# Kernel tuning notes

Measured on AMD Instinct MI355X. Metric: run time of the kernel, lower is better.

The kernel has to match this reference:

```python
import jax, jax.numpy as jnp
import numpy as np

B, S, H, I, E = 2, 2048, 1024, 4096, 8
NUM_STEPS = 2
RMS_EPS = 1e-6


def rmsnorm(x, w, eps=RMS_EPS):
    var = jnp.mean(jnp.square(x), axis=-1, keepdims=True)
    return x * jax.lax.rsqrt(var + eps) * w


def setup_inputs() -> dict:
    key = jax.random.key(0)
    ks = jax.random.split(key, 7)
    return {
        "hidden_states": jax.random.normal(ks[0], (B, S, H), dtype=jnp.float32),
        "gate_w": jax.random.normal(ks[1], (E, H), dtype=jnp.float32) * 0.02,
        "w1": jax.random.normal(ks[2], (E, H, I), dtype=jnp.float32) * 0.02,
        "b1": jnp.zeros((E, I), dtype=jnp.float32),
        "w2": jax.random.normal(ks[3], (E, I, H), dtype=jnp.float32) * 0.02,
        "b2": jnp.zeros((E, H), dtype=jnp.float32),
        "ln_w": jnp.ones((H,), dtype=jnp.float32),
    }


def reference(hidden_states, gate_w, w1, b1, w2, b2, ln_w):
    x = hidden_states  # [B,S,H]
    dtype = hidden_states.dtype
    for i in range(NUM_STEPS):
        inp = x if i == 0 else rmsnorm(x, ln_w)
        t = inp.reshape(-1, H)  # [T,H], T = B*S
        # softmax gate (computed in fp32 as in the original)
        logits = t @ gate_w.T  # [T,E]
        rw = jax.nn.softmax(logits.astype(jnp.float32), axis=-1).astype(dtype)
        # all experts on all tokens (dense MoE), batched over E
        h = jax.nn.silu(jnp.einsum('td,edi->tei', t, w1) + b1)  # [T,E,I]
        eo = jnp.einsum('tei,eih->teh', h, w2) + b2             # [T,E,H]
        comb = jnp.einsum('te,teh->th', rw, eo)                 # weighted combine
        x = x + comb.reshape(B, S, H)
    return x  # final_projection is Identity (no feature extractor)
```

## Files before the change

### kernel.cpp

```cpp
#include <hip/hip_runtime.h>
#include <hip/hip_bf16.h>

#define T_TOK 4096
#define H_DIM 1024
#define I_DIM 4096
#define E_EXP 8
#define RMS_EPS_F 1e-6f

using bf16x8 = __attribute__((ext_vector_type(8))) __bf16;
using f32x4  = __attribute__((ext_vector_type(4))) float;

__device__ inline void gload_lds16(const void* g, void* l) {
    __builtin_amdgcn_global_load_lds(
        (const __attribute__((address_space(1))) void*)g,
        (__attribute__((address_space(3))) void*)l,
        16, 0, 0);
}

__global__ __launch_bounds__(256) void k_transpose_cvt(
    const float* __restrict__ in, __hip_bfloat16* __restrict__ out, int R, int C)
{
    __shared__ float tile[32][33];
    const size_t mat = (size_t)R * C;
    in  += (size_t)blockIdx.z * mat;
    out += (size_t)blockIdx.z * mat;
    const int c0 = blockIdx.x * 32, r0 = blockIdx.y * 32;
    const int tx = threadIdx.x & 31, ty = threadIdx.x >> 5;
#pragma unroll
    for (int dy = 0; dy < 32; dy += 8)
        tile[ty + dy][tx] = in[(size_t)(r0 + ty + dy) * C + (c0 + tx)];
    __syncthreads();
#pragma unroll
    for (int dy = 0; dy < 32; dy += 8)
        out[(size_t)(c0 + ty + dy) * R + (r0 + tx)] = __float2bfloat16(tile[tx][ty + dy]);
}

__global__ __launch_bounds__(256) void k_prep(
    const float* __restrict__ x, const float* __restrict__ lnw,
    __hip_bfloat16* __restrict__ tb, int do_norm)
{
    const int t = blockIdx.x;
    const float* row = x + (size_t)t * H_DIM;
    const int base = threadIdx.x * 4;
    float4 v = *(const float4*)(row + base);
    if (do_norm) {
        float ss = v.x*v.x + v.y*v.y + v.z*v.z + v.w*v.w;
#pragma unroll
        for (int off = 32; off > 0; off >>= 1) ss += __shfl_xor(ss, off);
        __shared__ float wsum[4];
        const int w = threadIdx.x >> 6;
        if ((threadIdx.x & 63) == 0) wsum[w] = ss;
        __syncthreads();
        const float tot = wsum[0] + wsum[1] + wsum[2] + wsum[3];
        const float scale = rsqrtf(tot * (1.0f / H_DIM) + RMS_EPS_F);
        float4 g = *(const float4*)(lnw + base);
        v.x *= scale * g.x; v.y *= scale * g.y; v.z *= scale * g.z; v.w *= scale * g.w;
    }
    __hip_bfloat16* o = tb + (size_t)t * H_DIM + base;
    o[0] = __float2bfloat16(v.x); o[1] = __float2bfloat16(v.y);
    o[2] = __float2bfloat16(v.z); o[3] = __float2bfloat16(v.w);
}

__global__ __launch_bounds__(256) void k_gate(
    const __hip_bfloat16* __restrict__ tb, const float* __restrict__ gw,
    float* __restrict__ rw)
{
    const int t = blockIdx.x * 4 + (threadIdx.x >> 6);
    const int lane = threadIdx.x & 63;
    const __hip_bfloat16* row = tb + (size_t)t * H_DIM;
    float acc[E_EXP];
#pragma unroll
    for (int e = 0; e < E_EXP; ++e) acc[e] = 0.f;
    for (int h = lane; h < H_DIM; h += 64) {
        const float xv = __bfloat162float(row[h]);
#pragma unroll
        for (int e = 0; e < E_EXP; ++e) acc[e] += xv * gw[e * H_DIM + h];
    }
#pragma unroll
    for (int e = 0; e < E_EXP; ++e) {
#pragma unroll
        for (int off = 32; off > 0; off >>= 1) acc[e] += __shfl_xor(acc[e], off);
    }
    if (lane == 0) {
        float mx = acc[0];
#pragma unroll
        for (int e = 1; e < E_EXP; ++e) mx = fmaxf(mx, acc[e]);
        float ex[E_EXP], s = 0.f;
#pragma unroll
        for (int e = 0; e < E_EXP; ++e) { ex[e] = __expf(acc[e] - mx); s += ex[e]; }
        const float inv = 1.f / s;
#pragma unroll
        for (int e = 0; e < E_EXP; ++e) rw[(size_t)t * E_EXP + e] = ex[e] * inv;
    }
}


template<int BB, int MBASE>
__device__ __forceinline__ void ld_a4(bf16x8 (&a)[4], const char* rdA, int kof) {
#pragma unroll
    for (int mi = 0; mi < 4; ++mi)
        a[mi] = *(const bf16x8*)(rdA + BB * 32768 + (MBASE + mi) * 2048 + kof);
}
template<int BB>
__device__ __forceinline__ void ld_b4(bf16x8 (&b)[4], const char* rdB, int kof) {
#pragma unroll
    for (int ni = 0; ni < 4; ++ni)
        b[ni] = *(const bf16x8*)(rdB + BB * 32768 + ni * 2048 + kof);
}
template<int MB>
__device__ __forceinline__ void mfma_cell(const bf16x8 (&a)[4], const bf16x8 (&b)[4],
                                          f32x4 (&acc)[8][4]) {
    __builtin_amdgcn_s_setprio(1);
#pragma unroll
    for (int mi = 0; mi < 4; ++mi)
#pragma unroll
        for (int ni = 0; ni < 4; ++ni)
            acc[MB + mi][ni] = __builtin_amdgcn_mfma_f32_16x16x32_bf16(
                a[mi], b[ni], acc[MB + mi][ni], 0, 0, 0);
    __builtin_amdgcn_s_setprio(0);
}

#define BAR()   __builtin_amdgcn_s_barrier()
#define LGKM0() asm volatile("s_waitcnt lgkmcnt(0)" ::: "memory")
#define VMW(n)  asm volatile("s_waitcnt vmcnt(" #n ")" ::: "memory")
#define SCHED0() __builtin_amdgcn_sched_barrier(0)

template <int MODE>
__global__ __launch_bounds__(512, 2) void k_gemm8(
    const __hip_bfloat16* __restrict__ A, int lda, long long strideA,
    const __hip_bfloat16* __restrict__ Bt, int ldb, long long strideB,
    const float* __restrict__ bias, int strideBias,
    const float* __restrict__ rw, int e0,
    void* __restrict__ out, int ldo, long long strideOut, int K)
{
    __shared__ __hip_bfloat16 sA[2][2][128 * 64];
    __shared__ __hip_bfloat16 sB[2][2][128 * 64];

    const int z = blockIdx.z;
    A  += (size_t)z * (size_t)strideA;
    Bt += (size_t)z * (size_t)strideB;

    const int tid  = threadIdx.x;
    const int lane = tid & 63;
    const int wid  = tid >> 6;
    const int wr = wid >> 2, wc = wid & 3;
    const int m0 = blockIdx.y * 256, n0 = blockIdx.x * 256;

    const int sr  = tid >> 3;
    const int skb = ((((tid & 7) * 16) ^ ((sr & 7) << 4)) >> 1);
    const __hip_bfloat16* gA = A  + (size_t)(m0 + sr) * lda + skb;
    const __hip_bfloat16* gB = Bt + (size_t)(n0 + sr) * ldb + skb;
    char* const dA = (char*)&sA[0][0][0] + tid * 16;
    char* const dB = (char*)&sB[0][0][0] + tid * 16;

#define STAGE_A(bb, hh, kt) do { \
    const __hip_bfloat16* s_ = gA + (size_t)(hh) * 128 * lda + (size_t)(kt) * 64; \
    gload_lds16(s_,                     dA + (bb) * 32768 + (hh) * 16384); \
    gload_lds16(s_ + (size_t)64 * lda,  dA + (bb) * 32768 + (hh) * 16384 + 8192); \
} while (0)
#define STAGE_B(bb, hh, kt) do { \
    const __hip_bfloat16* s_ = gB + (size_t)(hh) * 128 * ldb + (size_t)(kt) * 64; \
    gload_lds16(s_,                     dB + (bb) * 32768 + (hh) * 16384); \
    gload_lds16(s_ + (size_t)64 * ldb,  dB + (bb) * 32768 + (hh) * 16384 + 8192); \
} while (0)

    const int fr = lane & 15, kg = lane >> 4;
    const int msk  = (fr & 7) << 4;
    const int kof0 = (kg * 16) ^ msk;
    const int kof1 = (64 + kg * 16) ^ msk;
    const char* rdA = (const char*)&sA[0][wr][0] + fr * 128;
    const char* rdB = (const char*)&sB[0][wc >> 1][0] + (wc & 1) * 8192 + fr * 128;

    f32x4  acc[8][4] = {};
    bf16x8 a[4], b[4], a2[4], a2n[4], bn[4];

    const int NT = K >> 6;

    STAGE_B(0, 0, 0); STAGE_B(0, 1, 0);
    STAGE_A(0, 0, 0); STAGE_A(0, 1, 0);
    STAGE_B(1, 0, 1); STAGE_B(1, 1, 1);
    VMW(4); BAR(); SCHED0();

#define TILE_PIPE(BB, t) do { \
     \
    ld_a4<BB, 0>(a, rdA, kof0); \
    ld_b4<BB>(b, rdB, kof0); \
    STAGE_A((BB) ^ 1, 0, (t) + 1); \
    LGKM0(); SCHED0(); \
    ld_a4<BB, 4>(a2, rdA, kof0);             \
    SCHED0(); \
    mfma_cell<0>(a, b, acc); \
     \
    STAGE_A((BB) ^ 1, 1, (t) + 1); \
    LGKM0(); SCHED0(); \
    ld_a4<BB, 4>(a2n, rdA, kof1);            \
    ld_b4<BB>(bn, rdB, kof1); \
    SCHED0(); \
    mfma_cell<4>(a2, b, acc); \
    BAR();                                    \
     \
    LGKM0(); SCHED0(); \
    ld_a4<BB, 0>(a, rdA, kof1);              \
    SCHED0(); \
    STAGE_B(BB, 0, (t) + 2); \
    mfma_cell<4>(a2n, bn, acc); \
     \
    LGKM0(); SCHED0(); \
    STAGE_B(BB, 1, (t) + 2); \
    mfma_cell<0>(a, bn, acc); \
    VMW(4); BAR(); SCHED0(); \
} while (0)

    for (int i = 0; i < NT / 2 - 1; ++i) {
        TILE_PIPE(0, 2 * i);
        TILE_PIPE(1, 2 * i + 1);
    }
    {
        ld_a4<0, 0>(a, rdA, kof0);
        ld_b4<0>(b, rdB, kof0);
        STAGE_A(1, 0, NT - 1);
        LGKM0(); SCHED0();
        ld_a4<0, 4>(a2, rdA, kof0);
        SCHED0();
        mfma_cell<0>(a, b, acc);
        STAGE_A(1, 1, NT - 1);
        LGKM0(); SCHED0();
        ld_a4<0, 4>(a2n, rdA, kof1);
        ld_b4<0>(bn, rdB, kof1);
        SCHED0();
        mfma_cell<4>(a2, b, acc);
        BAR();
        LGKM0(); SCHED0();
        ld_a4<0, 0>(a, rdA, kof1);
        SCHED0();
        mfma_cell<4>(a2n, bn, acc);
        LGKM0(); SCHED0();
        mfma_cell<0>(a, bn, acc);
        VMW(0); BAR(); SCHED0();
        ld_a4<1, 0>(a, rdA, kof0);
        ld_b4<1>(b, rdB, kof0);
        LGKM0(); SCHED0();
        ld_a4<1, 4>(a2, rdA, kof0);
        SCHED0();
        mfma_cell<0>(a, b, acc);
        LGKM0(); SCHED0();
        ld_a4<1, 4>(a2n, rdA, kof1);
        ld_b4<1>(bn, rdB, kof1);
        SCHED0();
        mfma_cell<4>(a2, b, acc);
        LGKM0(); SCHED0();
        ld_a4<1, 0>(a, rdA, kof1);
        SCHED0();
        mfma_cell<4>(a2n, bn, acc);
        LGKM0(); SCHED0();
        mfma_cell<0>(a, bn, acc);
    }

    const int rB = kg * 4;
    if (MODE == 0) {
        __hip_bfloat16* O = (__hip_bfloat16*)out + (size_t)z * (size_t)strideOut;
        const float* bz = bias + (size_t)z * (size_t)strideBias;
#pragma unroll
        for (int mi = 0; mi < 8; ++mi) {
            const int gm = m0 + wr * 128 + mi * 16 + rB;
#pragma unroll
            for (int j = 0; j < 4; ++j) {
                const int row = gm + j;
                const float rwv = rw[(size_t)row * E_EXP + e0 + z];
#pragma unroll
                for (int ni = 0; ni < 4; ++ni) {
                    const int gn = n0 + wc * 64 + ni * 16 + fr;
                    float v = acc[mi][ni][j] + bz[gn];
                    v = v / (1.f + __expf(-v));
                    O[(size_t)row * ldo + gn] = __float2bfloat16(rwv * v);
                }
            }
        }
    } else {
        __hip_bfloat16* O = (__hip_bfloat16*)out + (size_t)z * (size_t)strideOut;
#pragma unroll
        for (int mi = 0; mi < 8; ++mi) {
            const int gm = m0 + wr * 128 + mi * 16 + rB;
#pragma unroll
            for (int ni = 0; ni < 4; ++ni) {
                const int gn = n0 + wc * 64 + ni * 16 + fr;
#pragma unroll
                for (int j = 0; j < 4; ++j)
                    O[(size_t)(gm + j) * ldo + gn] = __float2bfloat16(acc[mi][ni][j]);
            }
        }
    }
#undef STAGE_A
#undef STAGE_B
#undef TILE_PIPE
}

__global__ __launch_bounds__(256) void k_combine(
    const __hip_bfloat16* __restrict__ eo, const float* __restrict__ rw,
    const float* __restrict__ b2, float* __restrict__ x, int e0, int g)
{
    const int t = blockIdx.x;
    const int h = threadIdx.x * 4;
    float4 acc = *(const float4*)(x + (size_t)t * H_DIM + h);
    for (int j = 0; j < g; ++j) {
        const float w = rw[(size_t)t * E_EXP + e0 + j];
        const __hip_bfloat16* p = eo + ((size_t)j * T_TOK + t) * H_DIM + h;
        const float4 bz = *(const float4*)(b2 + (size_t)(e0 + j) * H_DIM + h);
        acc.x += __bfloat162float(p[0]) + w * bz.x;
        acc.y += __bfloat162float(p[1]) + w * bz.y;
        acc.z += __bfloat162float(p[2]) + w * bz.z;
        acc.w += __bfloat162float(p[3]) + w * bz.w;
    }
    *(float4*)(x + (size_t)t * H_DIM + h) = acc;
}

extern "C" void kernel_launch(void* const* d_in, const int* in_sizes, int n_in,
                              void* d_out, int out_size, void* d_ws, size_t ws_size,
                              hipStream_t stream)
{
    const float* hidden = (const float*)d_in[0];
    const float* gate_w = (const float*)d_in[1];
    const float* w1     = (const float*)d_in[2];
    const float* b1     = (const float*)d_in[3];
    const float* w2     = (const float*)d_in[4];
    const float* b2     = (const float*)d_in[5];
    const float* ln_w   = (const float*)d_in[6];
    float* x = (float*)d_out;

    const size_t w1t_b = (size_t)E_EXP * I_DIM * H_DIM * 2;
    const size_t w2t_b = (size_t)E_EXP * H_DIM * I_DIM * 2;
    const size_t tb_b  = (size_t)T_TOK * H_DIM * 2;
    const size_t rw_b  = (size_t)T_TOK * E_EXP * 4;
    const size_t hb1_b = (size_t)T_TOK * I_DIM * 2;
    const size_t eo1_b = (size_t)T_TOK * H_DIM * 2;
    const size_t base_b = w1t_b + w2t_b + tb_b + rw_b;

    int g = 0;
    for (int cand = 8; cand >= 1; cand >>= 1)
        if (base_b + (size_t)cand * (hb1_b + eo1_b) <= ws_size) { g = cand; break; }

    char* ws = (char*)d_ws;
    __hip_bfloat16* w1t = (__hip_bfloat16*)ws;  ws += w1t_b;
    __hip_bfloat16* w2t = (__hip_bfloat16*)ws;  ws += w2t_b;
    __hip_bfloat16* tb  = (__hip_bfloat16*)ws;  ws += tb_b;
    float*          rw  = (float*)ws;           ws += rw_b;
    __hip_bfloat16* hb  = (__hip_bfloat16*)ws;
    __hip_bfloat16* eo  = (__hip_bfloat16*)(ws + (size_t)(g > 0 ? g : 1) * hb1_b);

    hipMemcpyAsync(x, hidden, (size_t)T_TOK * H_DIM * 4, hipMemcpyDeviceToDevice, stream);

    if (g == 0) return;

    k_transpose_cvt<<<dim3(I_DIM / 32, H_DIM / 32, E_EXP), 256, 0, stream>>>(w1, w1t, H_DIM, I_DIM);
    k_transpose_cvt<<<dim3(H_DIM / 32, I_DIM / 32, E_EXP), 256, 0, stream>>>(w2, w2t, I_DIM, H_DIM);

    for (int step = 0; step < 2; ++step) {
        k_prep<<<T_TOK, 256, 0, stream>>>(x, ln_w, tb, step);
        k_gate<<<T_TOK / 4, 256, 0, stream>>>(tb, gate_w, rw);

        for (int e0 = 0; e0 < E_EXP; e0 += g) {
            k_gemm8<0><<<dim3(I_DIM / 256, T_TOK / 256, g), 512, 0, stream>>>(
                tb, H_DIM, 0,
                w1t + (size_t)e0 * I_DIM * H_DIM, H_DIM, (long long)I_DIM * H_DIM,
                b1 + (size_t)e0 * I_DIM, I_DIM,
                rw, e0,
                hb, I_DIM, (long long)T_TOK * I_DIM, H_DIM);
            k_gemm8<2><<<dim3(H_DIM / 256, T_TOK / 256, g), 512, 0, stream>>>(
                hb, I_DIM, (long long)T_TOK * I_DIM,
                w2t + (size_t)e0 * H_DIM * I_DIM, I_DIM, (long long)H_DIM * I_DIM,
                nullptr, 0,
                nullptr, 0,
                eo, H_DIM, (long long)T_TOK * H_DIM, I_DIM);
            k_combine<<<T_TOK, 256, 0, stream>>>(eo, rw, b2, x, e0, g);
        }
    }
}
```

Measured before the change: 1.430 ms.

## Make expert GEMMs persistent and prefetch next tile during epilogue

Turns the batched expert GEMM into a persistent kernel with at most 256 workgroups. Each workgroup loops over several output tiles and issues the global-to-LDS staging for the next tile before running the current tile's epilogue stores. The aim is to hide prologue and epilogue latency and cut launch tail effects. Tile counts must divide evenly by the grid (rounds = tiles/grid), and the order in which tiles are assigned changes cache locality.

```diff
diff --git a/kernel.cpp b/kernel.cpp
--- a/kernel.cpp
+++ b/kernel.cpp
@@ -126,32 +126,51 @@
 #define SCHED0() __builtin_amdgcn_sched_barrier(0)
 
 template <int MODE>
-__global__ __launch_bounds__(512, 2) void k_gemm8(
+__global__ __launch_bounds__(512, 2) void k_gemm8p(
     const __hip_bfloat16* __restrict__ A, int lda, long long strideA,
     const __hip_bfloat16* __restrict__ Bt, int ldb, long long strideB,
     const float* __restrict__ bias, int strideBias,
     const float* __restrict__ rw, int e0,
-    void* __restrict__ out, int ldo, long long strideOut, int K)
+    void* __restrict__ out, int ldo, long long strideOut, int K,
+    int gx, int gy, int rounds)
 {
     __shared__ __hip_bfloat16 sA[2][2][128 * 64];
     __shared__ __hip_bfloat16 sB[2][2][128 * 64];
-
-    const int z = blockIdx.z;
-    A  += (size_t)z * (size_t)strideA;
-    Bt += (size_t)z * (size_t)strideB;
 
     const int tid  = threadIdx.x;
     const int lane = tid & 63;
     const int wid  = tid >> 6;
     const int wr = wid >> 2, wc = wid & 3;
-    const int m0 = blockIdx.y * 256, n0 = blockIdx.x * 256;
 
     const int sr  = tid >> 3;
     const int skb = ((((tid & 7) * 16) ^ ((sr & 7) << 4)) >> 1);
-    const __hip_bfloat16* gA = A  + (size_t)(m0 + sr) * lda + skb;
-    const __hip_bfloat16* gB = Bt + (size_t)(n0 + sr) * ldb + skb;
     char* const dA = (char*)&sA[0][0][0] + tid * 16;
     char* const dB = (char*)&sB[0][0][0] + tid * 16;
+
+    const int fr = lane & 15, kg = lane >> 4;
+    const int msk  = (fr & 7) << 4;
+    const int kof0 = (kg * 16) ^ msk;
+    const int kof1 = (64 + kg * 16) ^ msk;
+    const char* rdA = (const char*)&sA[0][wr][0] + fr * 128;
+    const char* rdB = (const char*)&sB[0][wc >> 1][0] + (wc & 1) * 8192 + fr * 128;
+
+    const int NT = K >> 6;
+    const int rB = kg * 4;
+
+    const __hip_bfloat16* gA;
+    const __hip_bfloat16* gB;
+    int m0, n0, zz;
+
+#define SET_TILE(r) do { \
+    const int idx_ = blockIdx.x + (r) * gridDim.x; \
+    const int x_ = idx_ % gx; \
+    const int t2_ = idx_ / gx; \
+    const int y_ = t2_ % gy; \
+    zz = t2_ / gy; \
+    m0 = y_ * 256; n0 = x_ * 256; \
+    gA = A + (size_t)zz * (size_t)strideA + (size_t)(m0 + sr) * lda + skb; \
+    gB = Bt + (size_t)zz * (size_t)strideB + (size_t)(n0 + sr) * ldb + skb; \
+} while (0)
 
 #define STAGE_A(bb, hh, kt) do { \
     const __hip_bfloat16* s_ = gA + (size_t)(hh) * 128 * lda + (size_t)(kt) * 64; \
@@ -164,58 +183,58 @@
     gload_lds16(s_ + (size_t)64 * ldb,  dB + (bb) * 32768 + (hh) * 16384 + 8192); \
 } while (0)
 
-    const int fr = lane & 15, kg = lane >> 4;
-    const int msk  = (fr & 7) << 4;
-    const int kof0 = (kg * 16) ^ msk;
-    const int kof1 = (64 + kg * 16) ^ msk;
-    const char* rdA = (const char*)&sA[0][wr][0] + fr * 128;
-    const char* rdB = (const char*)&sB[0][wc >> 1][0] + (wc & 1) * 8192 + fr * 128;
-
-    f32x4  acc[8][4] = {};
-    bf16x8 a[4], b[4], a2[4], a2n[4], bn[4];
-
-    const int NT = K >> 6;
-
-    STAGE_B(0, 0, 0); STAGE_B(0, 1, 0);
-    STAGE_A(0, 0, 0); STAGE_A(0, 1, 0);
-    STAGE_B(1, 0, 1); STAGE_B(1, 1, 1);
-    VMW(4); BAR(); SCHED0();
+#define STAGE12() do { \
+    STAGE_B(0, 0, 0); STAGE_B(0, 1, 0); \
+    STAGE_A(0, 0, 0); STAGE_A(0, 1, 0); \
+    STAGE_B(1, 0, 1); STAGE_B(1, 1, 1); \
+} while (0)
 
 #define TILE_PIPE(BB, t) do { \
-     \
     ld_a4<BB, 0>(a, rdA, kof0); \
     ld_b4<BB>(b, rdB, kof0); \
     STAGE_A((BB) ^ 1, 0, (t) + 1); \
     LGKM0(); SCHED0(); \
-    ld_a4<BB, 4>(a2, rdA, kof0);             \
+    ld_a4<BB, 4>(a2, rdA, kof0); \
     SCHED0(); \
     mfma_cell<0>(a, b, acc); \
-     \
     STAGE_A((BB) ^ 1, 1, (t) + 1); \
     LGKM0(); SCHED0(); \
-    ld_a4<BB, 4>(a2n, rdA, kof1);            \
+    ld_a4<BB, 4>(a2n, rdA, kof1); \
     ld_b4<BB>(bn, rdB, kof1); \
     SCHED0(); \
     mfma_cell<4>(a2, b, acc); \
-    BAR();                                    \
-     \
+    BAR(); \
     LGKM0(); SCHED0(); \
-    ld_a4<BB, 0>(a, rdA, kof1);              \
+    ld_a4<BB, 0>(a, rdA, kof1); \
     SCHED0(); \
     STAGE_B(BB, 0, (t) + 2); \
     mfma_cell<4>(a2n, bn, acc); \
-     \
     LGKM0(); SCHED0(); \
     STAGE_B(BB, 1, (t) + 2); \
     mfma_cell<0>(a, bn, acc); \
     VMW(4); BAR(); SCHED0(); \
 } while (0)
 
-    for (int i = 0; i < NT / 2 - 1; ++i) {
-        TILE_PIPE(0, 2 * i);
-        TILE_PIPE(1, 2 * i + 1);
-    }
-    {
+    f32x4  acc[8][4];
+    bf16x8 a[4], b[4], a2[4], a2n[4], bn[4];
+
+    SET_TILE(0);
+    STAGE12();
+
+#pragma unroll 1
+    for (int r = 0; r < rounds; ++r) {
+        VMW(4); BAR(); SCHED0();
+#pragma unroll
+        for (int mi = 0; mi < 8; ++mi)
+#pragma unroll
+            for (int ni = 0; ni < 4; ++ni)
+#pragma unroll
+                for (int q = 0; q < 4; ++q) acc[mi][ni][q] = 0.f;
+
+        for (int i = 0; i < NT / 2 - 1; ++i) {
+            TILE_PIPE(0, 2 * i);
+            TILE_PIPE(1, 2 * i + 1);
+        }
         ld_a4<0, 0>(a, rdA, kof0);
         ld_b4<0>(b, rdB, kof0);
         STAGE_A(1, 0, NT - 1);
@@ -254,44 +273,49 @@
         mfma_cell<4>(a2n, bn, acc);
         LGKM0(); SCHED0();
         mfma_cell<0>(a, bn, acc);
-    }
-
-    const int rB = kg * 4;
-    if (MODE == 0) {
-        __hip_bfloat16* O = (__hip_bfloat16*)out + (size_t)z * (size_t)strideOut;
-        const float* bz = bias + (size_t)z * (size_t)strideBias;
-#pragma unroll
-        for (int mi = 0; mi < 8; ++mi) {
-            const int gm = m0 + wr * 128 + mi * 16 + rB;
-#pragma unroll
-            for (int j = 0; j < 4; ++j) {
-                const int row = gm + j;
-                const float rwv = rw[(size_t)row * E_EXP + e0 + z];
+
+        BAR();
+        const int em0 = m0, en0 = n0, ez = zz;
+        if (r + 1 < rounds) { SET_TILE(r + 1); STAGE12(); }
+
+        if (MODE == 0) {
+            __hip_bfloat16* O = (__hip_bfloat16*)out + (size_t)ez * (size_t)strideOut;
+            const float* bz = bias + (size_t)ez * (size_t)strideBias;
+#pragma unroll
+            for (int mi = 0; mi < 8; ++mi) {
+                const int gm = em0 + wr * 128 + mi * 16 + rB;
+#pragma unroll
+                for (int j = 0; j < 4; ++j) {
+                    const int row = gm + j;
+                    const float rwv = rw[(size_t)row * E_EXP + e0 + ez];
+#pragma unroll
+                    for (int ni = 0; ni < 4; ++ni) {
+                        const int gn = en0 + wc * 64 + ni * 16 + fr;
+                        float v = acc[mi][ni][j] + bz[gn];
+                        v = v / (1.f + __expf(-v));
+                        O[(size_t)row * ldo + gn] = __float2bfloat16(rwv * v);
+                    }
+                }
+            }
+        } else {
+            __hip_bfloat16* O = (__hip_bfloat16*)out + (size_t)ez * (size_t)strideOut;
+#pragma unroll
+            for (int mi = 0; mi < 8; ++mi) {
+                const int gm = em0 + wr * 128 + mi * 16 + rB;
 #pragma unroll
                 for (int ni = 0; ni < 4; ++ni) {
-                    const int gn = n0 + wc * 64 + ni * 16 + fr;
-                    float v = acc[mi][ni][j] + bz[gn];
-                    v = v / (1.f + __expf(-v));
-                    O[(size_t)row * ldo + gn] = __float2bfloat16(rwv * v);
+                    const int gn = en0 + wc * 64 + ni * 16 + fr;
+#pragma unroll
+                    for (int j = 0; j < 4; ++j)
+                        O[(size_t)(gm + j) * ldo + gn] = __float2bfloat16(acc[mi][ni][j]);
                 }
             }
         }
-    } else {
-        __hip_bfloat16* O = (__hip_bfloat16*)out + (size_t)z * (size_t)strideOut;
-#pragma unroll
-        for (int mi = 0; mi < 8; ++mi) {
-            const int gm = m0 + wr * 128 + mi * 16 + rB;
-#pragma unroll
-            for (int ni = 0; ni < 4; ++ni) {
-                const int gn = n0 + wc * 64 + ni * 16 + fr;
-#pragma unroll
-                for (int j = 0; j < 4; ++j)
-                    O[(size_t)(gm + j) * ldo + gn] = __float2bfloat16(acc[mi][ni][j]);
-            }
-        }
-    }
+    }
+#undef SET_TILE
 #undef STAGE_A
 #undef STAGE_B
+#undef STAGE12
 #undef TILE_PIPE
 }
 
@@ -359,18 +383,26 @@
         k_gate<<<T_TOK / 4, 256, 0, stream>>>(tb, gate_w, rw);
 
         for (int e0 = 0; e0 < E_EXP; e0 += g) {
-            k_gemm8<0><<<dim3(I_DIM / 256, T_TOK / 256, g), 512, 0, stream>>>(
+            const int gx1 = I_DIM / 256, gy1 = T_TOK / 256;
+            const int tiles1 = gx1 * gy1 * g;
+            const int grid1  = tiles1 < 256 ? tiles1 : 256;
+            k_gemm8p<0><<<grid1, 512, 0, stream>>>(
                 tb, H_DIM, 0,
                 w1t + (size_t)e0 * I_DIM * H_DIM, H_DIM, (long long)I_DIM * H_DIM,
                 b1 + (size_t)e0 * I_DIM, I_DIM,
                 rw, e0,
-                hb, I_DIM, (long long)T_TOK * I_DIM, H_DIM);
-            k_gemm8<2><<<dim3(H_DIM / 256, T_TOK / 256, g), 512, 0, stream>>>(
+                hb, I_DIM, (long long)T_TOK * I_DIM, H_DIM,
+                gx1, gy1, tiles1 / grid1);
+            const int gx2 = H_DIM / 256, gy2 = T_TOK / 256;
+            const int tiles2 = gx2 * gy2 * g;
+            const int grid2  = tiles2 < 256 ? tiles2 : 256;
+            k_gemm8p<2><<<grid2, 512, 0, stream>>>(
                 hb, I_DIM, (long long)T_TOK * I_DIM,
                 w2t + (size_t)e0 * H_DIM * I_DIM, I_DIM, (long long)H_DIM * I_DIM,
                 nullptr, 0,
                 nullptr, 0,
-                eo, H_DIM, (long long)T_TOK * H_DIM, I_DIM);
+                eo, H_DIM, (long long)T_TOK * H_DIM, I_DIM,
+                gx2, gy2, tiles2 / grid2);
             k_combine<<<T_TOK, 256, 0, stream>>>(eo, rw, b2, x, e0, g);
         }
     }
```

New measurement: 1.434 ms. Within noise of the previous version (+0.3%).

## Restructure GEMM K-loop into two 32-MFMA phases per tile

Applied to the files above, without the earlier changes.

Replaces the four-cell interleaved LDS-load/MFMA pipeline with two larger phases per K tile. Each phase loads all 8 A fragments plus both halves of B, then issues 32 MFMAs, with extra barriers around the stages. This is meant to cut lgkm waits and scheduling barriers and give longer uninterrupted MFMA runs. In exchange it uses more registers at once, makes the barrier placement coarser, and loses some overlap of LDS reads with MFMA work.

```diff
diff --git a/kernel.cpp b/kernel.cpp
--- a/kernel.cpp
+++ b/kernel.cpp
@@ -95,28 +95,30 @@
 }
 
 
-template<int BB, int MBASE>
-__device__ __forceinline__ void ld_a4(bf16x8 (&a)[4], const char* rdA, int kof) {
-#pragma unroll
-    for (int mi = 0; mi < 4; ++mi)
-        a[mi] = *(const bf16x8*)(rdA + BB * 32768 + (MBASE + mi) * 2048 + kof);
-}
 template<int BB>
-__device__ __forceinline__ void ld_b4(bf16x8 (&b)[4], const char* rdB, int kof) {
-#pragma unroll
-    for (int ni = 0; ni < 4; ++ni)
-        b[ni] = *(const bf16x8*)(rdB + BB * 32768 + ni * 2048 + kof);
-}
-template<int MB>
-__device__ __forceinline__ void mfma_cell(const bf16x8 (&a)[4], const bf16x8 (&b)[4],
-                                          f32x4 (&acc)[8][4]) {
+__device__ __forceinline__ void ld_a8(bf16x8 (&a)[8], const char* rdA, int kof) {
+#pragma unroll
+    for (int mi = 0; mi < 8; ++mi)
+        a[mi] = *(const bf16x8*)(rdA + BB * 32768 + mi * 2048 + kof);
+}
+template<int BB>
+__device__ __forceinline__ void ld_b8(bf16x8 (&b)[8], const char* rdB, int kof0, int kof1) {
+#pragma unroll
+    for (int ni = 0; ni < 4; ++ni) {
+        b[ni]     = *(const bf16x8*)(rdB + BB * 32768 + ni * 2048 + kof0);
+        b[ni + 4] = *(const bf16x8*)(rdB + BB * 32768 + ni * 2048 + kof1);
+    }
+}
+template<int KC>
+__device__ __forceinline__ void mfma32(const bf16x8 (&a)[8], const bf16x8 (&b)[8],
+                                       f32x4 (&acc)[8][4]) {
     __builtin_amdgcn_s_setprio(1);
 #pragma unroll
-    for (int mi = 0; mi < 4; ++mi)
+    for (int mi = 0; mi < 8; ++mi)
 #pragma unroll
         for (int ni = 0; ni < 4; ++ni)
-            acc[MB + mi][ni] = __builtin_amdgcn_mfma_f32_16x16x32_bf16(
-                a[mi], b[ni], acc[MB + mi][ni], 0, 0, 0);
+            acc[mi][ni] = __builtin_amdgcn_mfma_f32_16x16x32_bf16(
+                a[mi], b[KC * 4 + ni], acc[mi][ni], 0, 0, 0);
     __builtin_amdgcn_s_setprio(0);
 }
 
@@ -172,7 +174,7 @@
     const char* rdB = (const char*)&sB[0][wc >> 1][0] + (wc & 1) * 8192 + fr * 128;
 
     f32x4  acc[8][4] = {};
-    bf16x8 a[4], b[4], a2[4], a2n[4], bn[4];
+    bf16x8 a[8], b[8];
 
     const int NT = K >> 6;
 
@@ -181,79 +183,42 @@
     STAGE_B(1, 0, 1); STAGE_B(1, 1, 1);
     VMW(4); BAR(); SCHED0();
 
-#define TILE_PIPE(BB, t) do { \
-     \
-    ld_a4<BB, 0>(a, rdA, kof0); \
-    ld_b4<BB>(b, rdB, kof0); \
-    STAGE_A((BB) ^ 1, 0, (t) + 1); \
+#define TILE2(BB, t) do { \
+    ld_a8<BB>(a, rdA, kof0); \
+    ld_b8<BB>(b, rdB, kof0, kof1); \
+    STAGE_A((BB) ^ 1, 0, (t) + 1); STAGE_A((BB) ^ 1, 1, (t) + 1); \
+    BAR(); LGKM0(); SCHED0(); \
+    mfma32<0>(a, b, acc); \
+    BAR(); \
+    ld_a8<BB>(a, rdA, kof1); \
+    STAGE_B(BB, 0, (t) + 2); STAGE_B(BB, 1, (t) + 2); \
     LGKM0(); SCHED0(); \
-    ld_a4<BB, 4>(a2, rdA, kof0);             \
-    SCHED0(); \
-    mfma_cell<0>(a, b, acc); \
-     \
-    STAGE_A((BB) ^ 1, 1, (t) + 1); \
-    LGKM0(); SCHED0(); \
-    ld_a4<BB, 4>(a2n, rdA, kof1);            \
-    ld_b4<BB>(bn, rdB, kof1); \
-    SCHED0(); \
-    mfma_cell<4>(a2, b, acc); \
-    BAR();                                    \
-     \
-    LGKM0(); SCHED0(); \
-    ld_a4<BB, 0>(a, rdA, kof1);              \
-    SCHED0(); \
-    STAGE_B(BB, 0, (t) + 2); \
-    mfma_cell<4>(a2n, bn, acc); \
-     \
-    LGKM0(); SCHED0(); \
-    STAGE_B(BB, 1, (t) + 2); \
-    mfma_cell<0>(a, bn, acc); \
+    mfma32<1>(a, b, acc); \
     VMW(4); BAR(); SCHED0(); \
 } while (0)
 
     for (int i = 0; i < NT / 2 - 1; ++i) {
-        TILE_PIPE(0, 2 * i);
-        TILE_PIPE(1, 2 * i + 1);
+        TILE2(0, 2 * i);
+        TILE2(1, 2 * i + 1);
     }
     {
-        ld_a4<0, 0>(a, rdA, kof0);
-        ld_b4<0>(b, rdB, kof0);
-        STAGE_A(1, 0, NT - 1);
+        ld_a8<0>(a, rdA, kof0);
+        ld_b8<0>(b, rdB, kof0, kof1);
+        STAGE_A(1, 0, NT - 1); STAGE_A(1, 1, NT - 1);
+        BAR(); LGKM0(); SCHED0();
+        mfma32<0>(a, b, acc);
+        BAR();
+        ld_a8<0>(a, rdA, kof1);
         LGKM0(); SCHED0();
-        ld_a4<0, 4>(a2, rdA, kof0);
-        SCHED0();
-        mfma_cell<0>(a, b, acc);
-        STAGE_A(1, 1, NT - 1);
+        mfma32<1>(a, b, acc);
+        VMW(0); BAR(); SCHED0();
+        ld_a8<1>(a, rdA, kof0);
+        ld_b8<1>(b, rdB, kof0, kof1);
         LGKM0(); SCHED0();
-        ld_a4<0, 4>(a2n, rdA, kof1);
-        ld_b4<0>(bn, rdB, kof1);
-        SCHED0();
-        mfma_cell<4>(a2, b, acc);
-        BAR();
+        mfma32<0>(a, b, acc);
+        ld_a8<1>(a, rdA, kof1);
         LGKM0(); SCHED0();
-        ld_a4<0, 0>(a, rdA, kof1);
-        SCHED0();
-        mfma_cell<4>(a2n, bn, acc);
-        LGKM0(); SCHED0();
-        mfma_cell<0>(a, bn, acc);
-        VMW(0); BAR(); SCHED0();
-        ld_a4<1, 0>(a, rdA, kof0);
-        ld_b4<1>(b, rdB, kof0);
-        LGKM0(); SCHED0();
-        ld_a4<1, 4>(a2, rdA, kof0);
-        SCHED0();
-        mfma_cell<0>(a, b, acc);
-        LGKM0(); SCHED0();
-        ld_a4<1, 4>(a2n, rdA, kof1);
-        ld_b4<1>(bn, rdB, kof1);
-        SCHED0();
-        mfma_cell<4>(a2, b, acc);
-        LGKM0(); SCHED0();
-        ld_a4<1, 0>(a, rdA, kof1);
-        SCHED0();
-        mfma_cell<4>(a2n, bn, acc);
-        LGKM0(); SCHED0();
-        mfma_cell<0>(a, bn, acc);
+        mfma32<1>(a, b, acc);
     }
 
     const int rB = kg * 4;
@@ -292,7 +257,7 @@
     }
 #undef STAGE_A
 #undef STAGE_B
-#undef TILE_PIPE
+#undef TILE2
 }
 
 __global__ __launch_bounds__(256) void k_combine(
```

After: 1.503 ms. +5.1%, slower.
